# Performance work log

Hardware: AMD Instinct MI355X
Metric: run time of the kernel (lower is better)

Reference implementation:

```python
import jax, jax.numpy as jnp
import numpy as np


def setup_inputs() -> dict:
    key = jax.random.key(0)
    k1, k2, k3 = jax.random.split(key, 3)
    B, D, N, C = 4096, 256, 65536, 10
    x = jax.random.normal(k1, (B, D), dtype=jnp.float32)
    keys = jax.random.normal(k2, (N, D), dtype=jnp.float32)
    values = jax.random.uniform(k3, (N, C), dtype=jnp.float32)
    return {"x": x, "keys": keys, "values": values, "k": 8}


def reference(x, keys, values, k):
    # squared euclidean distances [B, N] without materializing diff cube:
    x_sq = jnp.sum(x * x, axis=1, keepdims=True)          # [B,1]
    k_sq = jnp.sum(keys * keys, axis=1)                   # [N]
    dists = x_sq - 2.0 * (x @ keys.T) + k_sq[None, :]     # [B,N]
    neg_top, indices = jax.lax.top_k(-dists, k)           # [B,k]
    hit_values = values[indices]                          # [B,k,C]
    return jnp.sum(hit_values, axis=1) / jnp.float32(k)   # [B,C]
```

## Files before the change

### kernel.cpp

```cpp
#include <hip/hip_runtime.h>
#include <stdint.h>
#include <float.h>

#define B_ROWS 4096
#define N_KEYS 65536
#define DDIM 256
#define NCH 10

#define NSPLIT 16
#define SPLIT_KEYS (N_KEYS / NSPLIT)
#define ROWS_PER_BLK 128
#define CHUNK_KEYS 64
#define NCHUNK (SPLIT_KEYS / CHUNK_KEYS)

typedef float f32x4 __attribute__((ext_vector_type(4)));
typedef float f32x16 __attribute__((ext_vector_type(16)));
typedef short bf16x8 __attribute__((ext_vector_type(8)));

static __device__ __forceinline__ unsigned short f2bf(float f) {
  unsigned u = __float_as_uint(f);
  return (unsigned short)((u + 0x7FFFu + ((u >> 16) & 1u)) >> 16);
}
static __device__ __forceinline__ unsigned ford(float f) {
  unsigned u = __float_as_uint(f);
  return u ^ ((unsigned)((int)u >> 31) | 0x80000000u);
}
static __device__ __forceinline__ unsigned long long shfl_xor_u64(unsigned long long v, int m) {
  unsigned lo = __shfl_xor((unsigned)v, m, 64);
  unsigned hi = __shfl_xor((unsigned)(v >> 32), m, 64);
  return ((unsigned long long)hi << 32) | lo;
}
static __device__ __forceinline__ double shfl_xor_f64(double v, int m) {
  return __longlong_as_double((long long)shfl_xor_u64((unsigned long long)__double_as_longlong(v), m));
}
static __device__ __forceinline__ void gl_lds16(const void* g, void* l) {
  __builtin_amdgcn_global_load_lds(
      (const __attribute__((address_space(1))) unsigned int*)g,
      (__attribute__((address_space(3))) unsigned int*)l, 16, 0, 0);
}

__global__ __launch_bounds__(256) void transpose_keys(const float* __restrict__ keys,
                                                      unsigned char* __restrict__ kbf,
                                                      float* __restrict__ ksq) {
  __shared__ __align__(16) unsigned char T[128 * 512];
  const int t = threadIdx.x;
  const int lane = t & 63;
  const float4* src = (const float4*)(keys + (size_t)blockIdx.x * 128 * DDIM);
#pragma unroll
  for (int j = 0; j < 32; ++j) {
    int g = j * 256 + t;
    float4 v = src[g];
    int key = g >> 6;
    int u = lane >> 1, sub = lane & 1;
    unsigned lo = ((unsigned)f2bf(v.y) << 16) | f2bf(v.x);
    unsigned hi2 = ((unsigned)f2bf(v.w) << 16) | f2bf(v.z);
    unsigned long long p = ((unsigned long long)hi2 << 32) | lo;
    *(unsigned long long*)&T[key * 512 + ((u ^ (key & 7)) << 4) + (sub << 3)] = p;
    float ss = v.x * v.x + v.y * v.y + v.z * v.z + v.w * v.w;
#pragma unroll
    for (int off = 32; off; off >>= 1) ss += __shfl_xor(ss, off, 64);
    if (lane == 0) ksq[blockIdx.x * 128 + key] = ss;
  }
  __syncthreads();
  uint4* dst = (uint4*)kbf + (size_t)blockIdx.x * 4096;
#pragma unroll
  for (int j = 0; j < 16; ++j) {
    int ou = j * 256 + t;
    int rec = ou >> 10, rem = ou & 1023;
    int koct = rem >> 5, key32 = rem & 31;
    int keyl = rec * 32 + key32;
    dst[ou] = *(const uint4*)&T[keyl * 512 + ((koct ^ (keyl & 7)) << 4)];
  }
}

__global__ __launch_bounds__(512, 4) void knn_main(
    const float* __restrict__ x,
    const unsigned char* __restrict__ kbf,
    const float* __restrict__ ksqg,
    unsigned int* __restrict__ pools,
    unsigned int* __restrict__ counts,
    int CAP) {
  __shared__ __align__(16) unsigned char tiles[2][32768];
  __shared__ float tauh[2][4][32];
  __shared__ unsigned int rowcnt[128];

  const int t = threadIdx.x;
  const int lane = t & 63;
  const int wv = t >> 6;
  const int mw = wv & 1;
  const int ws = wv >> 1;
  const int col = lane & 31;
  const int hi5 = lane >> 5;

  const int split = blockIdx.x & (NSPLIT - 1);
  const int rb = (blockIdx.x >> 4) * ROWS_PER_BLK;
  const int sb = split * SPLIT_KEYS;

  const int xrow = rb + ws * 32 + col;
  const int rl = ws * 32 + col;

  bf16x8 xb[16];
#pragma unroll
  for (int s = 0; s < 16; ++s) {
    const float* p = x + (size_t)xrow * DDIM + s * 16 + hi5 * 8;
    float4 a = *(const float4*)p, b = *(const float4*)(p + 4);
    union { unsigned short us[8]; bf16x8 v; } u;
    u.us[0]=f2bf(-2.f*a.x); u.us[1]=f2bf(-2.f*a.y); u.us[2]=f2bf(-2.f*a.z); u.us[3]=f2bf(-2.f*a.w);
    u.us[4]=f2bf(-2.f*b.x); u.us[5]=f2bf(-2.f*b.y); u.us[6]=f2bf(-2.f*b.z); u.us[7]=f2bf(-2.f*b.w);
    xb[s] = u.v;
  }

  if (t < 128) rowcnt[t] = 0;

  float sminA = FLT_MAX, sminB = FLT_MAX;
  const unsigned char* srcbase = kbf + (size_t)sb * 512;
  const size_t pb = ((size_t)xrow * NSPLIT + split) * (size_t)CAP;

  auto STAGE = [&](int c, int buf) {
    const unsigned char* src = srcbase + ((size_t)c << 15);
#pragma unroll
    for (int i = 0; i < 4; ++i)
      gl_lds16(src + (((i * 512) + t) << 4),
               (unsigned char*)tiles[buf] + ((i * 512 + wv * 64) << 4));
  };

  f32x16 acc;

  auto COMPUTE = [&](int c, int buf) {
    const float* kq = ksqg + sb + c * CHUNK_KEYS + mw * 32 + hi5 * 4;
    float4 q0 = *(const float4*)(kq);
    float4 q1 = *(const float4*)(kq + 8);
    float4 q2 = *(const float4*)(kq + 16);
    float4 q3 = *(const float4*)(kq + 24);
    acc[0]=q0.x; acc[1]=q0.y; acc[2]=q0.z; acc[3]=q0.w;
    acc[4]=q1.x; acc[5]=q1.y; acc[6]=q1.z; acc[7]=q1.w;
    acc[8]=q2.x; acc[9]=q2.y; acc[10]=q2.z; acc[11]=q2.w;
    acc[12]=q3.x; acc[13]=q3.y; acc[14]=q3.z; acc[15]=q3.w;
    const unsigned char* rec = tiles[buf] + mw * 16384 + col * 16;
    __builtin_amdgcn_s_setprio(1);
#pragma unroll
    for (int s = 0; s < 16; ++s) {
      bf16x8 af = *(const bf16x8*)(rec + (2 * s + hi5) * 512);
      acc = __builtin_amdgcn_mfma_f32_32x32x16_bf16(af, xb[s], acc, 0, 0, 0);
    }
    __builtin_amdgcn_s_setprio(0);
  };

  auto SEL = [&](int c, bool append, float tau) {
    float m0 = fminf(fminf(fminf(acc[0], acc[1]), fminf(acc[2], acc[3])),
                     fminf(fminf(acc[4], acc[5]), fminf(acc[6], acc[7])));
    float m1 = fminf(fminf(fminf(acc[8], acc[9]), fminf(acc[10], acc[11])),
                     fminf(fminf(acc[12], acc[13]), fminf(acc[14], acc[15])));
    sminA = fminf(sminA, m0);
    sminB = fminf(sminB, m1);
    if (append && fminf(m0, m1) <= tau) {
      const int kbase = c * CHUNK_KEYS + mw * 32 + 4 * hi5;
#pragma unroll
      for (int r = 0; r < 16; ++r) {
        float sc = acc[r];
        if (sc <= tau) {
          int key = kbase + (r & 3) + 8 * (r >> 2);
          unsigned slot = atomicAdd(&rowcnt[rl], 1u);
          if ((int)slot < CAP)
            pools[pb + slot] = (ford(sc) & 0xFFFFF000u) | (unsigned)key;
        }
      }
    }
  };

  auto PUBLISH = [&]() {
    float l = fmaxf(sminA, sminB);
    l = fmaxf(l, __shfl_xor(l, 32, 64));
    if (hi5 == 0) tauh[mw][ws][col] = l;
  };
  auto RDTAU = [&]() {
    return fmaxf(tauh[0][ws][col], tauh[1][ws][col]);
  };

  STAGE(0, 0);
  STAGE(32, 1);
  __syncthreads();
  COMPUTE(0, 0);  SEL(0, false, 0.f);
  COMPUTE(32, 1); SEL(32, false, 0.f);
  PUBLISH();
  __syncthreads();

#pragma unroll 1
  for (int c = 0; c < NCHUNK; ++c) {
    asm volatile("s_waitcnt vmcnt(4)" ::: "memory");
    __builtin_amdgcn_s_barrier();
    const int cs = (c + 1 < NCHUNK) ? c + 1 : 0;
    STAGE(cs, (c + 1) & 1);
    float tau = RDTAU();
    COMPUTE(c, c & 1);
    SEL(c, true, tau);
    if (c & 1) PUBLISH();
  }

  __syncthreads();
  if (t < 128) counts[(size_t)(rb + t) * NSPLIT + split] = rowcnt[t];
}

__global__ __launch_bounds__(64) void knn_refine(
    const float* __restrict__ x,
    const float* __restrict__ keys,
    const float* __restrict__ ksq,
    const float* __restrict__ values,
    const unsigned int* __restrict__ pools,
    const unsigned int* __restrict__ counts,
    int CAP,
    float* __restrict__ out) {
  __shared__ float4 xl[64];
  const int row = blockIdx.x;
  const int lane = threadIdx.x;

  xl[lane] = ((const float4*)(x + (size_t)row * DDIM))[lane];
  __syncthreads();

  unsigned long long h[8];
#pragma unroll
  for (int i = 0; i < 8; ++i) h[i] = ~0ULL;

  auto insert = [&](unsigned long long v) {
    if (v < h[7]) {
#pragma unroll
      for (int j = 7; j >= 1; --j) {
        unsigned long long a = h[j - 1];
        unsigned long long mx = a > v ? a : v;
        h[j] = (v < h[j]) ? mx : h[j];
      }
      h[0] = h[0] < v ? h[0] : v;
    }
  };

  for (int s = 0; s < NSPLIT; ++s) {
    unsigned cnt = counts[(size_t)row * NSPLIT + s];
    if ((int)cnt <= CAP) {
      const unsigned int* pp = pools + ((size_t)row * NSPLIT + s) * (size_t)CAP;
      for (int i = lane; i < (int)cnt; i += 64) {
        unsigned p = pp[i];
        unsigned gk = (unsigned)(s * SPLIT_KEYS) + (p & 0xFFFu);
        insert(((unsigned long long)(p & 0xFFFFF000u) << 16) | gk);
      }
    } else {
      for (int kk = lane; kk < SPLIT_KEYS; kk += 64) {
        int gk = s * SPLIT_KEYS + kk;
        const float4* kr = (const float4*)(keys + (size_t)gk * DDIM);
        float acc = 0.f;
#pragma unroll 8
        for (int d = 0; d < 64; ++d) {
          float4 kv = kr[d], xv = xl[d];
          acc = fmaf(kv.x, xv.x, acc); acc = fmaf(kv.y, xv.y, acc);
          acc = fmaf(kv.z, xv.z, acc); acc = fmaf(kv.w, xv.w, acc);
        }
        float sc = fmaf(-2.0f, acc, ksq[gk]);
        insert(((unsigned long long)(ford(sc) & 0xFFFFF000u) << 16) | (unsigned)gk);
      }
    }
  }

  int myidx = 0;
#pragma unroll 1
  for (int r = 0; r < 24; ++r) {
    unsigned long long m = h[0];
#pragma unroll
    for (int off = 32; off; off >>= 1) {
      unsigned long long o = shfl_xor_u64(m, off);
      m = o < m ? o : m;
    }
    if (lane == r) myidx = (int)(m & 0xFFFFu);
    if (h[0] == m) {
#pragma unroll
      for (int i = 0; i < 7; ++i) h[i] = h[i + 1];
      h[7] = ~0ULL;
    }
  }

  double dv = 1e300;
  if (lane < 24) {
    const float4* kr = (const float4*)(keys + (size_t)myidx * DDIM);
    double s = 0.0;
#pragma unroll 8
    for (int d = 0; d < 64; ++d) {
      float4 kv = kr[d], xv = xl[d];
      double d0 = (double)xv.x - (double)kv.x;
      double d1 = (double)xv.y - (double)kv.y;
      double d2 = (double)xv.z - (double)kv.z;
      double d3 = (double)xv.w - (double)kv.w;
      s += d0 * d0 + d1 * d1 + d2 * d2 + d3 * d3;
    }
    dv = s;
  }

  int di = myidx;
  int chosen[8];
#pragma unroll
  for (int r = 0; r < 8; ++r) {
    double m = dv; int mi = di;
#pragma unroll
    for (int off = 32; off; off >>= 1) {
      double om = shfl_xor_f64(m, off);
      int omi = __shfl_xor(mi, off, 64);
      if (om < m || (om == m && omi < mi)) { m = om; mi = omi; }
    }
    chosen[r] = mi;
    if (di == mi && dv < 1e300) dv = 1e300;
  }

  if (lane < NCH) {
    double a = 0.0;
#pragma unroll
    for (int r = 0; r < 8; ++r) a += (double)values[(size_t)chosen[r] * NCH + lane];
    out[row * NCH + lane] = (float)(a * 0.125);
  }
}

extern "C" void kernel_launch(void* const* d_in, const int* in_sizes, int n_in,
                              void* d_out, int out_size, void* d_ws, size_t ws_size,
                              hipStream_t stream) {
  (void)in_sizes; (void)n_in; (void)out_size;
  const float* x      = (const float*)d_in[0];
  const float* keys   = (const float*)d_in[1];
  const float* values = (const float*)d_in[2];
  float* out = (float*)d_out;

  char* ws = (char*)d_ws;
  unsigned char* kbf = (unsigned char*)ws;
  float* ksq   = (float*)(ws + 33554432);
  unsigned int* counts = (unsigned int*)(ws + 33554432 + 262144);
  unsigned int* pools  = (unsigned int*)(ws + 33554432 + 262144 + 262144);

  size_t base = 33554432 + 262144 + 262144;
  size_t cap = (ws_size > base) ? (ws_size - base) / ((size_t)B_ROWS * NSPLIT * 4) : 60;
  if (cap < 60) cap = 60;
  if (cap > 512) cap = 512;
  int CAP = (int)cap;

  transpose_keys<<<N_KEYS / 128, 256, 0, stream>>>(keys, kbf, ksq);
  knn_main<<<(B_ROWS / ROWS_PER_BLK) * NSPLIT, 512, 0, stream>>>(
      x, kbf, ksq, pools, counts, CAP);
  knn_refine<<<B_ROWS, 64, 0, stream>>>(x, keys, ksq, values, pools, counts, CAP, out);
}
```

Baseline: 302.2 us.

## Pack key norms into staged tiles and split MFMA accumulator chain

The transpose kernel now writes each 64-key chunk record with its squared norms appended, so the main kernel stages norms into LDS together with the bf16 keys instead of loading them from global memory in the compute step. The MFMA reduction is split into two independent accumulators that are summed with the norms afterward, which shortens the dependent MFMA chain. In exchange, the wait count becomes vmcnt(0) because of the extra load, which removes some load/compute overlap, and the record stride grows slightly (33792 bytes), so the staged tiles are no longer power-of-two aligned.

```diff
diff --git a/kernel.cpp b/kernel.cpp
--- a/kernel.cpp
+++ b/kernel.cpp
@@ -12,6 +12,7 @@
 #define ROWS_PER_BLK 128
 #define CHUNK_KEYS 64
 #define NCHUNK (SPLIT_KEYS / CHUNK_KEYS)
+#define RECB 33792
 
 typedef float f32x4 __attribute__((ext_vector_type(4)));
 typedef float f32x16 __attribute__((ext_vector_type(16)));
@@ -43,6 +44,7 @@
                                                       unsigned char* __restrict__ kbf,
                                                       float* __restrict__ ksq) {
   __shared__ __align__(16) unsigned char T[128 * 512];
+  __shared__ float sq[128];
   const int t = threadIdx.x;
   const int lane = t & 63;
   const float4* src = (const float4*)(keys + (size_t)blockIdx.x * 128 * DDIM);
@@ -59,28 +61,31 @@
     float ss = v.x * v.x + v.y * v.y + v.z * v.z + v.w * v.w;
 #pragma unroll
     for (int off = 32; off; off >>= 1) ss += __shfl_xor(ss, off, 64);
-    if (lane == 0) ksq[blockIdx.x * 128 + key] = ss;
-  }
-  __syncthreads();
-  uint4* dst = (uint4*)kbf + (size_t)blockIdx.x * 4096;
+    if (lane == 0) { ksq[blockIdx.x * 128 + key] = ss; sq[key] = ss; }
+  }
+  __syncthreads();
+  unsigned char* rec0 = kbf + (size_t)(blockIdx.x * 2) * RECB;
 #pragma unroll
   for (int j = 0; j < 16; ++j) {
     int ou = j * 256 + t;
-    int rec = ou >> 10, rem = ou & 1023;
+    int sr = ou >> 10, rem = ou & 1023;
     int koct = rem >> 5, key32 = rem & 31;
-    int keyl = rec * 32 + key32;
-    dst[ou] = *(const uint4*)&T[keyl * 512 + ((koct ^ (keyl & 7)) << 4)];
-  }
+    int keyl = sr * 32 + key32;
+    unsigned char* dst = rec0 + (size_t)(sr >> 1) * RECB + (sr & 1) * 16384
+                       + ((koct * 32 + key32) << 4);
+    *(uint4*)dst = *(const uint4*)&T[keyl * 512 + ((koct ^ (keyl & 7)) << 4)];
+  }
+  if (t < 128)
+    *(float*)(rec0 + (size_t)(t >> 6) * RECB + 32768 + ((t & 63) << 2)) = sq[t];
 }
 
 __global__ __launch_bounds__(512, 4) void knn_main(
     const float* __restrict__ x,
     const unsigned char* __restrict__ kbf,
-    const float* __restrict__ ksqg,
     unsigned int* __restrict__ pools,
     unsigned int* __restrict__ counts,
     int CAP) {
-  __shared__ __align__(16) unsigned char tiles[2][32768];
+  __shared__ __align__(16) unsigned char tiles[2][RECB];
   __shared__ float tauh[2][4][32];
   __shared__ unsigned int rowcnt[128];
 
@@ -94,7 +99,6 @@
 
   const int split = blockIdx.x & (NSPLIT - 1);
   const int rb = (blockIdx.x >> 4) * ROWS_PER_BLK;
-  const int sb = split * SPLIT_KEYS;
 
   const int xrow = rb + ws * 32 + col;
   const int rl = ws * 32 + col;
@@ -113,56 +117,63 @@
   if (t < 128) rowcnt[t] = 0;
 
   float sminA = FLT_MAX, sminB = FLT_MAX;
-  const unsigned char* srcbase = kbf + (size_t)sb * 512;
+  const unsigned char* srcbase = kbf + (size_t)(split * NCHUNK) * RECB;
   const size_t pb = ((size_t)xrow * NSPLIT + split) * (size_t)CAP;
 
   auto STAGE = [&](int c, int buf) {
-    const unsigned char* src = srcbase + ((size_t)c << 15);
+    const unsigned char* src = srcbase + (size_t)c * RECB;
 #pragma unroll
     for (int i = 0; i < 4; ++i)
       gl_lds16(src + (((i * 512) + t) << 4),
                (unsigned char*)tiles[buf] + ((i * 512 + wv * 64) << 4));
-  };
-
-  f32x16 acc;
-
-  auto COMPUTE = [&](int c, int buf) {
-    const float* kq = ksqg + sb + c * CHUNK_KEYS + mw * 32 + hi5 * 4;
-    float4 q0 = *(const float4*)(kq);
-    float4 q1 = *(const float4*)(kq + 8);
-    float4 q2 = *(const float4*)(kq + 16);
-    float4 q3 = *(const float4*)(kq + 24);
-    acc[0]=q0.x; acc[1]=q0.y; acc[2]=q0.z; acc[3]=q0.w;
-    acc[4]=q1.x; acc[5]=q1.y; acc[6]=q1.z; acc[7]=q1.w;
-    acc[8]=q2.x; acc[9]=q2.y; acc[10]=q2.z; acc[11]=q2.w;
-    acc[12]=q3.x; acc[13]=q3.y; acc[14]=q3.z; acc[15]=q3.w;
+    if (wv == 0)
+      gl_lds16(src + 32768 + (lane << 4), (unsigned char*)tiles[buf] + 32768);
+  };
+
+  f32x16 a0, a1;
+
+  auto COMPUTE = [&](int buf) {
     const unsigned char* rec = tiles[buf] + mw * 16384 + col * 16;
+    a0 = 0.0f; a1 = 0.0f;
     __builtin_amdgcn_s_setprio(1);
 #pragma unroll
-    for (int s = 0; s < 16; ++s) {
-      bf16x8 af = *(const bf16x8*)(rec + (2 * s + hi5) * 512);
-      acc = __builtin_amdgcn_mfma_f32_32x32x16_bf16(af, xb[s], acc, 0, 0, 0);
+    for (int s = 0; s < 8; ++s) {
+      bf16x8 afA = *(const bf16x8*)(rec + (2 * s + hi5) * 512);
+      bf16x8 afB = *(const bf16x8*)(rec + (2 * (s + 8) + hi5) * 512);
+      a0 = __builtin_amdgcn_mfma_f32_32x32x16_bf16(afA, xb[s], a0, 0, 0, 0);
+      a1 = __builtin_amdgcn_mfma_f32_32x32x16_bf16(afB, xb[s + 8], a1, 0, 0, 0);
     }
     __builtin_amdgcn_s_setprio(0);
   };
 
-  auto SEL = [&](int c, bool append, float tau) {
-    float m0 = fminf(fminf(fminf(acc[0], acc[1]), fminf(acc[2], acc[3])),
-                     fminf(fminf(acc[4], acc[5]), fminf(acc[6], acc[7])));
-    float m1 = fminf(fminf(fminf(acc[8], acc[9]), fminf(acc[10], acc[11])),
-                     fminf(fminf(acc[12], acc[13]), fminf(acc[14], acc[15])));
+  auto SEL = [&](int c, int buf, bool append, float tau) {
+    const float* sqp = (const float*)(tiles[buf] + 32768) + mw * 32 + hi5 * 4;
+    float4 q0 = *(const float4*)(sqp);
+    float4 q1 = *(const float4*)(sqp + 8);
+    float4 q2 = *(const float4*)(sqp + 16);
+    float4 q3 = *(const float4*)(sqp + 24);
+    float sc[16];
+#pragma unroll
+    for (int i = 0; i < 4; ++i) {
+      sc[i]      = a0[i]      + a1[i]      + ((const float*)&q0)[i];
+      sc[4 + i]  = a0[4 + i]  + a1[4 + i]  + ((const float*)&q1)[i];
+      sc[8 + i]  = a0[8 + i]  + a1[8 + i]  + ((const float*)&q2)[i];
+      sc[12 + i] = a0[12 + i] + a1[12 + i] + ((const float*)&q3)[i];
+    }
+    float m0 = sc[0], m1 = sc[8];
+#pragma unroll
+    for (int r = 1; r < 8; ++r) { m0 = fminf(m0, sc[r]); m1 = fminf(m1, sc[8 + r]); }
     sminA = fminf(sminA, m0);
     sminB = fminf(sminB, m1);
     if (append && fminf(m0, m1) <= tau) {
       const int kbase = c * CHUNK_KEYS + mw * 32 + 4 * hi5;
 #pragma unroll
       for (int r = 0; r < 16; ++r) {
-        float sc = acc[r];
-        if (sc <= tau) {
+        if (sc[r] <= tau) {
           int key = kbase + (r & 3) + 8 * (r >> 2);
           unsigned slot = atomicAdd(&rowcnt[rl], 1u);
           if ((int)slot < CAP)
-            pools[pb + slot] = (ford(sc) & 0xFFFFF000u) | (unsigned)key;
+            pools[pb + slot] = (ford(sc[r]) & 0xFFFFF000u) | (unsigned)key;
         }
       }
     }
@@ -180,20 +191,20 @@
   STAGE(0, 0);
   STAGE(32, 1);
   __syncthreads();
-  COMPUTE(0, 0);  SEL(0, false, 0.f);
-  COMPUTE(32, 1); SEL(32, false, 0.f);
+  COMPUTE(0);  SEL(0, 0, false, 0.f);
+  COMPUTE(1);  SEL(32, 1, false, 0.f);
   PUBLISH();
   __syncthreads();
 
 #pragma unroll 1
   for (int c = 0; c < NCHUNK; ++c) {
-    asm volatile("s_waitcnt vmcnt(4)" ::: "memory");
+    asm volatile("s_waitcnt vmcnt(0)" ::: "memory");
     __builtin_amdgcn_s_barrier();
     const int cs = (c + 1 < NCHUNK) ? c + 1 : 0;
     STAGE(cs, (c + 1) & 1);
     float tau = RDTAU();
-    COMPUTE(c, c & 1);
-    SEL(c, true, tau);
+    COMPUTE(c & 1);
+    SEL(c, c & 1, true, tau);
     if (c & 1) PUBLISH();
   }
 
@@ -326,18 +337,19 @@
 
   char* ws = (char*)d_ws;
   unsigned char* kbf = (unsigned char*)ws;
-  float* ksq   = (float*)(ws + 33554432);
-  unsigned int* counts = (unsigned int*)(ws + 33554432 + 262144);
-  unsigned int* pools  = (unsigned int*)(ws + 33554432 + 262144 + 262144);
-
-  size_t base = 33554432 + 262144 + 262144;
-  size_t cap = (ws_size > base) ? (ws_size - base) / ((size_t)B_ROWS * NSPLIT * 4) : 60;
-  if (cap < 60) cap = 60;
+  size_t kbf_bytes = (size_t)1024 * RECB;
+  float* ksq = (float*)(ws + kbf_bytes);
+  unsigned int* counts = (unsigned int*)(ws + kbf_bytes + 262144);
+  unsigned int* pools  = (unsigned int*)(ws + kbf_bytes + 262144 + 262144);
+
+  size_t base = kbf_bytes + 262144 + 262144;
+  size_t cap = (ws_size > base) ? (ws_size - base) / ((size_t)B_ROWS * NSPLIT * 4) : 56;
+  if (cap < 56) cap = 56;
   if (cap > 512) cap = 512;
   int CAP = (int)cap;
 
   transpose_keys<<<N_KEYS / 128, 256, 0, stream>>>(keys, kbf, ksq);
   knn_main<<<(B_ROWS / ROWS_PER_BLK) * NSPLIT, 512, 0, stream>>>(
-      x, kbf, ksq, pools, counts, CAP);
+      x, kbf, pools, counts, CAP);
   knn_refine<<<B_ROWS, 64, 0, stream>>>(x, keys, ksq, values, pools, counts, CAP, out);
 }
```

Measured after the change: 332.0 us. 1.1x slower.
